# Kernel optimization log

Hardware: AMD Instinct MI355X
Metric: run time of the kernel (lower is better)

Reference implementation:

```python
import jax, jax.numpy as jnp
import numpy as np

V_WORD = 32000      # word vocab (dictionary.symbols minus specials)
NGRAM_VOCAB = 32001 # threshold top ngrams + UNK
DIM = 128
LATENT = 10000
NSPECIAL = 4
PAD_IDX = 1         # fairseq pad index
NG_PER_WORD = 26    # avg char-ngrams per word for n=4
B, T = 8, 1024


def setup_inputs() -> dict:
    key = jax.random.key(0)
    k1, k2, k3, k4, k5 = jax.random.split(key, 5)
    ngram_emb_weight = jax.random.normal(k1, (NGRAM_VOCAB, DIM), jnp.float32) * (DIM ** -0.5)
    latent_mat = jax.random.normal(k2, (LATENT, DIM), jnp.float32) * (LATENT ** -0.5)
    special_emb = jax.random.normal(k3, (NSPECIAL, DIM), jnp.float32) * (DIM ** -0.5)
    special_emb = special_emb.at[PAD_IDX].set(0.0)  # nn.init.constant_(special_emb[pad], 0)
    ngram_ids = jax.random.randint(k4, (V_WORD * NG_PER_WORD,), 0, NGRAM_VOCAB, jnp.int32)
    ngram_offsets = jnp.arange(V_WORD, dtype=jnp.int32) * NG_PER_WORD
    x = jax.random.randint(k5, (B, T), 0, NSPECIAL + V_WORD, jnp.int32)
    return {
        "ngram_emb_weight": ngram_emb_weight,
        "latent_mat": latent_mat,
        "special_emb": special_emb,
        "ngram_ids": ngram_ids,
        "ngram_offsets": ngram_offsets,
        "x": x,
    }


def reference(ngram_emb_weight, latent_mat, special_emb, ngram_ids, ngram_offsets, x):
    n_total = ngram_ids.shape[0]
    # EmbeddingBag(mode='sum'): segment-sum gathered ngram vectors per word
    seg = jnp.searchsorted(ngram_offsets, jnp.arange(n_total, dtype=ngram_offsets.dtype), side='right') - 1
    bag = jax.ops.segment_sum(ngram_emb_weight[ngram_ids], seg, num_segments=V_WORD)  # [V_WORD, DIM]
    lang_emb = jnp.tanh(bag)
    # softmax attention over the latent codebook
    latent_scores = jnp.einsum('vd,ld->vl', lang_emb, latent_mat)          # [V_WORD, LATENT]
    latent_distribution = jax.nn.softmax(latent_scores, axis=-1)
    latent_emb = jnp.einsum('vl,ld->vd', latent_distribution, latent_mat)  # [V_WORD, DIM]
    token_emb = lang_emb + latent_emb
    emb_weight = jnp.concatenate([special_emb, token_emb], axis=0)          # [NSPECIAL+V_WORD, DIM]
    sde_emb = emb_weight[x]                                                 # [B, T, DIM]
    return sde_emb
```

## Files before the change

kernel.cpp:

```cpp
#include <hip/hip_runtime.h>

typedef float  f32x4 __attribute__((ext_vector_type(4)));
typedef short  s16x8 __attribute__((ext_vector_type(8)));
typedef int    i32x4 __attribute__((ext_vector_type(4)));
typedef unsigned short u16x4 __attribute__((ext_vector_type(4)));
typedef unsigned int   u32x2 __attribute__((ext_vector_type(2)));

#define V_WORD   32000
#define DIM      128
#define LATENT   10000
#define LATP     10048
#define NSPECIAL 4
#define NTOK     8192
#define NTILE    157
#define BN       64
#define K0_BLOCKS 314

__device__ __forceinline__ unsigned short f2bf(float f) {
  unsigned u = __builtin_bit_cast(unsigned, f);
  unsigned r = (u + 0x7fffu + ((u >> 16) & 1u)) >> 16;
  return (unsigned short)r;
}

__device__ __forceinline__ unsigned cvt_pk_bf16(float lo, float hi) {
  unsigned r;
  asm("v_cvt_pk_bf16_f32 %0, %1, %2" : "=v"(r) : "v"(lo), "v"(hi));
  return r;
}

__device__ __forceinline__ float tanh_fast(float x) {
  float t = __expf(2.f * x);
  return (t - 1.f) * __frcp_rn(t + 1.f);
}

__device__ __forceinline__ void gload_lds16(const void* g, void* l) {
  __builtin_amdgcn_global_load_lds(
      (const __attribute__((address_space(1))) void*)g,
      (__attribute__((address_space(3))) void*)l, 16, 0, 0);
}

__global__ __launch_bounds__(256) void k01_prep(
    const float* __restrict__ latent, unsigned short* __restrict__ Lb,
    unsigned short* __restrict__ LTb,
    const float* __restrict__ ngram_emb, const int* __restrict__ ids,
    const int* __restrict__ offs, const int* __restrict__ x,
    float* __restrict__ langf, unsigned short* __restrict__ langb) {
  __shared__ float tile[32][129];
  int bid = blockIdx.x;
  int tid = threadIdx.x;
  if (bid < K0_BLOCKS) {
    int l0 = bid * 32;
    int r  = tid >> 3;
    int c0 = (tid & 7) * 16;
    int l  = l0 + r;
    for (int k = 0; k < 4; ++k) {
      int d = c0 + k * 4;
      f32x4 v = {0.f, 0.f, 0.f, 0.f};
      if (l < LATENT) v = *reinterpret_cast<const f32x4*>(latent + (size_t)l * DIM + d);
      tile[r][d + 0] = v[0]; tile[r][d + 1] = v[1];
      tile[r][d + 2] = v[2]; tile[r][d + 3] = v[3];
      u16x4 o = { f2bf(v[0]), f2bf(v[1]), f2bf(v[2]), f2bf(v[3]) };
      *reinterpret_cast<u16x4*>(Lb + (size_t)l * DIM + d) = o;
    }
    __syncthreads();
    int d = tid >> 1;
    int lbase = (tid & 1) * 16;
    for (int k = 0; k < 8; ++k) {
      int ll = lbase + 2 * k;
      int l1 = l0 + ll;
      unsigned pack = (unsigned)f2bf(tile[ll][d]) | ((unsigned)f2bf(tile[ll + 1][d]) << 16);
      *reinterpret_cast<unsigned*>(LTb + (size_t)d * LATP + l1) = pack;
    }
  } else {
    int tok  = (bid - K0_BLOCKS) * 4 + (tid >> 6);
    int lane = tid & 63;
    int half = lane >> 5;
    int l32  = lane & 31;
    int w = x[tok];
    f32x4 s0 = {0.f, 0.f, 0.f, 0.f}, s1 = {0.f, 0.f, 0.f, 0.f};
    if (w >= NSPECIAL) {
      int base = offs[w - NSPECIAL];
#pragma unroll
      for (int j = 0; j < 24; j += 4) {
        int ia = ids[base + j + half];
        int ib = ids[base + j + 2 + half];
        s0 += *reinterpret_cast<const f32x4*>(ngram_emb + (size_t)ia * DIM + l32 * 4);
        s1 += *reinterpret_cast<const f32x4*>(ngram_emb + (size_t)ib * DIM + l32 * 4);
      }
      int ic = ids[base + 24 + half];
      s0 += *reinterpret_cast<const f32x4*>(ngram_emb + (size_t)ic * DIM + l32 * 4);
      s0 += s1;
      for (int c = 0; c < 4; ++c) s0[c] += __shfl_xor(s0[c], 32, 64);
      for (int c = 0; c < 4; ++c) s0[c] = tanh_fast(s0[c]);
    }
    if (half == 0) {
      *reinterpret_cast<f32x4*>(langf + (size_t)tok * DIM + l32 * 4) = s0;
    } else {
      u32x2 pw = { cvt_pk_bf16(s0[0], s0[1]), cvt_pk_bf16(s0[2], s0[3]) };
      *reinterpret_cast<u32x2*>(langb + (size_t)tok * DIM + l32 * 4) = pw;
    }
  }
}

__global__ __launch_bounds__(256, 2) void k2_fused(
    const unsigned short* __restrict__ Lb,
    const unsigned short* __restrict__ LTb,
    const unsigned short* __restrict__ langb,
    float* __restrict__ Opart,
    float* __restrict__ Zpart,
    int nsplit) {
  __shared__ alignas(16) unsigned short smem[5 * 8192];
  unsigned short* Psh = smem + 4 * 8192;
  float* zsh = (float*)Psh;

  int bid = blockIdx.x;
  int xcd = bid & 7, idx = bid >> 3;
  int split, tokblk;
  if (nsplit == 8)      { split = xcd;                   tokblk = idx; }
  else if (nsplit == 16){ split = xcd * 2 + (idx >> 6);  tokblk = idx & 63; }
  else                  { split = xcd >> 1;              tokblk = idx + ((xcd & 1) << 5); }
  int tokbase = tokblk * 128;
  int t0 = (split * NTILE) / nsplit, t1 = ((split + 1) * NTILE) / nsplit;
  int lat_s = t0 * BN;
  int ntiles = t1 - t0;
  int npad = max(0, t1 * BN - LATENT);

  int tid = threadIdx.x;
  int wid = tid >> 6, lane = tid & 63;
  int lr = lane & 15, lg = lane >> 4;
  int wm = wid & 1, wn = wid >> 1;

  int rL  = tid >> 4, csL = tid & 15;
  int coL = csL ^ (rL & 7);
  int ddT = tid >> 3, csT = tid & 7;
  int coT = csT ^ (ddT & 7);
  const unsigned short* srcL0 = Lb + (size_t)rL * DIM + coL * 8;
  const unsigned short* srcT0 = LTb + (size_t)ddT * LATP + coT * 8;
  int wbase = wid * 64 * 8;

  auto issue = [&](int buf, int t) {
    int lat0 = lat_s + t * BN;
    const unsigned short* sL = srcL0 + (size_t)lat0 * DIM;
    const unsigned short* sT = srcT0 + lat0;
    unsigned short* dL = smem + buf * 8192 + wbase;
    unsigned short* dT = smem + 16384 + buf * 8192 + wbase;
#pragma unroll
    for (int i = 0; i < 4; ++i)
      gload_lds16(sL + (size_t)i * 16 * DIM, dL + i * 2048);
#pragma unroll
    for (int i = 0; i < 4; ++i)
      gload_lds16(sT + (size_t)i * 32 * LATP, dT + i * 2048);
  };

  s16x8 Bl[4][4];
  for (int n = 0; n < 4; ++n) {
    int row = tokbase + wn * 64 + n * 16 + lr;
    for (int kf = 0; kf < 4; ++kf)
      Bl[n][kf] = *reinterpret_cast<const s16x8*>(langb + (size_t)row * DIM + (kf * 4 + lg) * 8);
  }

  f32x4 acc2[4][4];
  for (int a = 0; a < 4; ++a)
    for (int b = 0; b < 4; ++b) acc2[a][b] = {0.f, 0.f, 0.f, 0.f};
  float zp[4] = {0.f, 0.f, 0.f, 0.f};

  issue(0, 0);
  int cur = 0;

  for (int t = 0; t < ntiles; ++t) {
    asm volatile("s_waitcnt vmcnt(0)" ::: "memory");
    __syncthreads();
    if (t + 1 < ntiles) issue(cur ^ 1, t + 1);

    const unsigned short* Lsh  = smem + cur * 8192;
    const unsigned short* LTsh = smem + 16384 + cur * 8192;

    f32x4 acc1[2][4];
    for (int m = 0; m < 2; ++m)
      for (int n = 0; n < 4; ++n) acc1[m][n] = {0.f, 0.f, 0.f, 0.f};
    for (int kf = 0; kf < 4; ++kf) {
      s16x8 a[2];
      for (int m = 0; m < 2; ++m) {
        int row = wm * 32 + m * 16 + lr;
        int c = kf * 4 + lg;
        a[m] = *reinterpret_cast<const s16x8*>(&Lsh[row * DIM + (c ^ (row & 7)) * 8]);
      }
      __builtin_amdgcn_s_setprio(1);
      for (int m = 0; m < 2; ++m)
        for (int n = 0; n < 4; ++n)
          acc1[m][n] = __builtin_amdgcn_mfma_f32_16x16x32_bf16(a[m], Bl[n][kf], acc1[m][n], 0, 0, 0);
      __builtin_amdgcn_s_setprio(0);
    }

    for (int m = 0; m < 2; ++m) {
      int la0 = wm * 32 + m * 16 + lg * 4;
      for (int n = 0; n < 4; ++n) {
        f32x4 v = acc1[m][n];
        float p0 = __expf(v[0]), p1 = __expf(v[1]);
        float p2 = __expf(v[2]), p3 = __expf(v[3]);
        zp[n] += p0; zp[n] += p1; zp[n] += p2; zp[n] += p3;
        u32x2 pw = { cvt_pk_bf16(p0, p1), cvt_pk_bf16(p2, p3) };
        int row = wn * 64 + n * 16 + lr;
        int c = la0 >> 3;
        *reinterpret_cast<u32x2*>(&Psh[row * 64 + ((c ^ (row & 7)) << 3) + (la0 & 7)]) = pw;
      }
    }
    __syncthreads();

    for (int kf = 0; kf < 2; ++kf) {
      s16x8 Ap[4], Bt[4];
      int c = kf * 4 + lg;
      for (int mr = 0; mr < 4; ++mr) {
        int row = wm * 64 + mr * 16 + lr;
        Ap[mr] = *reinterpret_cast<const s16x8*>(&Psh[row * 64 + ((c ^ (row & 7)) << 3)]);
      }
      for (int nd = 0; nd < 4; ++nd) {
        int dr = wn * 64 + nd * 16 + lr;
        Bt[nd] = *reinterpret_cast<const s16x8*>(&LTsh[dr * 64 + ((c ^ (dr & 7)) << 3)]);
      }
      __builtin_amdgcn_s_setprio(1);
      for (int mr = 0; mr < 4; ++mr)
        for (int nd = 0; nd < 4; ++nd)
          acc2[mr][nd] = __builtin_amdgcn_mfma_f32_16x16x32_bf16(Ap[mr], Bt[nd], acc2[mr][nd], 0, 0, 0);
      __builtin_amdgcn_s_setprio(0);
    }
    cur ^= 1;
  }

  __syncthreads();

  for (int n = 0; n < 4; ++n) {
    zp[n] += __shfl_xor(zp[n], 16, 64);
    zp[n] += __shfl_xor(zp[n], 32, 64);
  }
  if (wm == 0 && lane < 16)
    for (int n = 0; n < 4; ++n) zsh[wn * 64 + n * 16 + lr] = zp[n];
  __syncthreads();
  if (wm == 1 && lane < 16)
    for (int n = 0; n < 4; ++n) zsh[wn * 64 + n * 16 + lr] += zp[n];
  __syncthreads();

  for (int mr = 0; mr < 4; ++mr) {
    int rbase = wm * 64 + mr * 16 + lg * 4;
    for (int nd = 0; nd < 4; ++nd) {
      int dcol = wn * 64 + nd * 16 + lr;
      for (int i = 0; i < 4; ++i) {
        int row = rbase + i;
        Opart[((size_t)split * NTOK + tokbase + row) * DIM + dcol] = acc2[mr][nd][i];
      }
    }
  }
  if (tid < 128)
    Zpart[split * NTOK + tokbase + tid] = zsh[tid] - (float)npad;
}

__global__ __launch_bounds__(256) void k3_combine(
    const float* __restrict__ special, const int* __restrict__ x,
    const float* __restrict__ langf, const float* __restrict__ Opart,
    const float* __restrict__ Zpart, float* __restrict__ out, int nsplit) {
  int gi  = blockIdx.x * 256 + threadIdx.x;
  int tok = gi >> 5;
  int d4  = (gi & 31) * 4;
  int w   = x[tok];
  f32x4 o;
  if (w < NSPECIAL) {
    o = *reinterpret_cast<const f32x4*>(special + (size_t)w * DIM + d4);
  } else {
    f32x4 s = {0.f, 0.f, 0.f, 0.f};
    float z = 0.f;
    for (int sp = 0; sp < nsplit; ++sp) {
      s += *reinterpret_cast<const f32x4*>(Opart + ((size_t)sp * NTOK + tok) * DIM + d4);
      z += Zpart[sp * NTOK + tok];
    }
    f32x4 lg = *reinterpret_cast<const f32x4*>(langf + (size_t)tok * DIM + d4);
    o = lg + s / z;
  }
  *reinterpret_cast<f32x4*>(out + (size_t)tok * DIM + d4) = o;
}

extern "C" void kernel_launch(void* const* d_in, const int* in_sizes, int n_in,
                              void* d_out, int out_size, void* d_ws, size_t ws_size,
                              hipStream_t stream) {
  const float* ngram_emb = (const float*)d_in[0];
  const float* latent    = (const float*)d_in[1];
  const float* special   = (const float*)d_in[2];
  const int*   ids       = (const int*)d_in[3];
  const int*   offs      = (const int*)d_in[4];
  const int*   x         = (const int*)d_in[5];
  float* out = (float*)d_out;

  size_t fixed = (size_t)LATP * DIM * 2 * 2
               + (size_t)NTOK * DIM * 4
               + (size_t)NTOK * DIM * 2;
  int nsplit = 8;
  while (nsplit > 4) {
    size_t need = fixed + (size_t)nsplit * NTOK * DIM * 4 + (size_t)nsplit * NTOK * 4;
    if (need <= ws_size) break;
    nsplit >>= 1;
  }

  char* w = (char*)d_ws;
  unsigned short* Lb  = (unsigned short*)w;  w += (size_t)LATP * DIM * 2;
  unsigned short* LTb = (unsigned short*)w;  w += (size_t)DIM * LATP * 2;
  float* langf        = (float*)w;           w += (size_t)NTOK * DIM * 4;
  unsigned short* langb = (unsigned short*)w; w += (size_t)NTOK * DIM * 2;
  float* Opart        = (float*)w;           w += (size_t)nsplit * NTOK * DIM * 4;
  float* Zpart        = (float*)w;           w += (size_t)nsplit * NTOK * 4;

  hipLaunchKernelGGL(k01_prep, dim3(K0_BLOCKS + NTOK / 4), dim3(256), 0, stream,
                     latent, Lb, LTb, ngram_emb, ids, offs, x, langf, langb);
  hipLaunchKernelGGL(k2_fused, dim3(nsplit * 64), dim3(256), 0, stream,
                     Lb, LTb, langb, Opart, Zpart, nsplit);
  hipLaunchKernelGGL(k3_combine, dim3(NTOK * DIM / 4 / 256), dim3(256), 0, stream,
                     special, x, langf, Opart, Zpart, out, nsplit);
}
```

Before: 140.6 us.

## Shrink LDS footprint to fit three blocks per CU and raise split count

```diff
diff --git a/kernel.cpp b/kernel.cpp
--- a/kernel.cpp
+++ b/kernel.cpp
@@ -102,22 +102,21 @@
   }
 }
 
-__global__ __launch_bounds__(256, 2) void k2_fused(
+__global__ __launch_bounds__(256, 3) void k2_fused(
     const unsigned short* __restrict__ Lb,
     const unsigned short* __restrict__ LTb,
     const unsigned short* __restrict__ langb,
     float* __restrict__ Opart,
     float* __restrict__ Zpart,
     int nsplit) {
-  __shared__ alignas(16) unsigned short smem[5 * 8192];
-  unsigned short* Psh = smem + 4 * 8192;
-  float* zsh = (float*)Psh;
+  __shared__ alignas(16) unsigned short smem[3 * 8192];
+  __shared__ float zsh[128];
 
   int bid = blockIdx.x;
   int xcd = bid & 7, idx = bid >> 3;
   int split, tokblk;
-  if (nsplit == 8)      { split = xcd;                   tokblk = idx; }
-  else if (nsplit == 16){ split = xcd * 2 + (idx >> 6);  tokblk = idx & 63; }
+  if (nsplit == 16)     { split = xcd * 2 + (idx >> 6);  tokblk = idx & 63; }
+  else if (nsplit == 8) { split = xcd;                   tokblk = idx; }
   else                  { split = xcd >> 1;              tokblk = idx + ((xcd & 1) << 5); }
   int tokbase = tokblk * 128;
   int t0 = (split * NTILE) / nsplit, t1 = ((split + 1) * NTILE) / nsplit;
@@ -136,20 +135,23 @@
   int coT = csT ^ (ddT & 7);
   const unsigned short* srcL0 = Lb + (size_t)rL * DIM + coL * 8;
   const unsigned short* srcT0 = LTb + (size_t)ddT * LATP + coT * 8;
-  int wbase = wid * 64 * 8;
-
-  auto issue = [&](int buf, int t) {
-    int lat0 = lat_s + t * BN;
-    const unsigned short* sL = srcL0 + (size_t)lat0 * DIM;
-    const unsigned short* sT = srcT0 + lat0;
-    unsigned short* dL = smem + buf * 8192 + wbase;
-    unsigned short* dT = smem + 16384 + buf * 8192 + wbase;
+  int wbase = wid * 512;
+
+  unsigned short* LTsh = smem + 16384;
+
+  auto issue_L = [&](int buf, int t) {
+    const unsigned short* s = srcL0 + (size_t)(lat_s + t * BN) * DIM;
+    unsigned short* d = smem + buf * 8192 + wbase;
 #pragma unroll
     for (int i = 0; i < 4; ++i)
-      gload_lds16(sL + (size_t)i * 16 * DIM, dL + i * 2048);
+      gload_lds16(s + (size_t)i * 16 * DIM, d + i * 2048);
+  };
+  auto issue_LT = [&](int t) {
+    const unsigned short* s = srcT0 + (lat_s + t * BN);
+    unsigned short* d = LTsh + wbase;
 #pragma unroll
     for (int i = 0; i < 4; ++i)
-      gload_lds16(sT + (size_t)i * 32 * LATP, dT + i * 2048);
+      gload_lds16(s + (size_t)i * 32 * LATP, d + i * 2048);
   };
 
   s16x8 Bl[4][4];
@@ -164,16 +166,17 @@
     for (int b = 0; b < 4; ++b) acc2[a][b] = {0.f, 0.f, 0.f, 0.f};
   float zp[4] = {0.f, 0.f, 0.f, 0.f};
 
-  issue(0, 0);
+  issue_L(0, 0);
   int cur = 0;
 
   for (int t = 0; t < ntiles; ++t) {
+    bool more = (t + 1 < ntiles);
     asm volatile("s_waitcnt vmcnt(0)" ::: "memory");
     __syncthreads();
-    if (t + 1 < ntiles) issue(cur ^ 1, t + 1);
-
-    const unsigned short* Lsh  = smem + cur * 8192;
-    const unsigned short* LTsh = smem + 16384 + cur * 8192;
+    issue_LT(t);
+    if (more) issue_L(cur ^ 1, t + 1);
+
+    const unsigned short* Lsh = smem + cur * 8192;
 
     f32x4 acc1[2][4];
     for (int m = 0; m < 2; ++m)
@@ -191,7 +194,9 @@
           acc1[m][n] = __builtin_amdgcn_mfma_f32_16x16x32_bf16(a[m], Bl[n][kf], acc1[m][n], 0, 0, 0);
       __builtin_amdgcn_s_setprio(0);
     }
-
+    __syncthreads();
+
+    unsigned short* Psh = smem + cur * 8192;
     for (int m = 0; m < 2; ++m) {
       int la0 = wm * 32 + m * 16 + lg * 4;
       for (int n = 0; n < 4; ++n) {
@@ -205,6 +210,8 @@
         *reinterpret_cast<u32x2*>(&Psh[row * 64 + ((c ^ (row & 7)) << 3) + (la0 & 7)]) = pw;
       }
     }
+    if (more) asm volatile("s_waitcnt vmcnt(4)" ::: "memory");
+    else      asm volatile("s_waitcnt vmcnt(0)" ::: "memory");
     __syncthreads();
 
     for (int kf = 0; kf < 2; ++kf) {
@@ -227,12 +234,11 @@
     cur ^= 1;
   }
 
-  __syncthreads();
-
   for (int n = 0; n < 4; ++n) {
     zp[n] += __shfl_xor(zp[n], 16, 64);
     zp[n] += __shfl_xor(zp[n], 32, 64);
   }
+  __syncthreads();
   if (wm == 0 && lane < 16)
     for (int n = 0; n < 4; ++n) zsh[wn * 64 + n * 16 + lr] = zp[n];
   __syncthreads();
@@ -292,7 +298,7 @@
   size_t fixed = (size_t)LATP * DIM * 2 * 2
                + (size_t)NTOK * DIM * 4
                + (size_t)NTOK * DIM * 2;
-  int nsplit = 8;
+  int nsplit = 16;
   while (nsplit > 4) {
     size_t need = fixed + (size_t)nsplit * NTOK * DIM * 4 + (size_t)nsplit * NTOK * 4;
     if (need <= ws_size) break;
```

Measured after the change: 213.8 us. 52.1% more time.

## Fuse split-K combine into GEMM kernel via last-block atomic counter, store partials bf16

Applied to the files above, without the earlier changes.

```diff
diff --git a/kernel.cpp b/kernel.cpp
--- a/kernel.cpp
+++ b/kernel.cpp
@@ -14,6 +14,7 @@
 #define NTOK     8192
 #define NTILE    157
 #define BN       64
+#define NSPLIT   8
 #define K0_BLOCKS 314
 
 __device__ __forceinline__ unsigned short f2bf(float f) {
@@ -31,6 +32,13 @@
 __device__ __forceinline__ float tanh_fast(float x) {
   float t = __expf(2.f * x);
   return (t - 1.f) * __frcp_rn(t + 1.f);
+}
+
+__device__ __forceinline__ float bfl(unsigned u) {
+  return __builtin_bit_cast(float, u << 16);
+}
+__device__ __forceinline__ float bfh(unsigned u) {
+  return __builtin_bit_cast(float, u & 0xffff0000u);
 }
 
 __device__ __forceinline__ void gload_lds16(const void* g, void* l) {
@@ -44,10 +52,12 @@
     unsigned short* __restrict__ LTb,
     const float* __restrict__ ngram_emb, const int* __restrict__ ids,
     const int* __restrict__ offs, const int* __restrict__ x,
-    float* __restrict__ langf, unsigned short* __restrict__ langb) {
+    float* __restrict__ langf, unsigned short* __restrict__ langb,
+    int* __restrict__ cnt) {
   __shared__ float tile[32][129];
   int bid = blockIdx.x;
   int tid = threadIdx.x;
+  if (bid == 0 && tid < 64) cnt[tid] = 0;
   if (bid < K0_BLOCKS) {
     int l0 = bid * 32;
     int r  = tid >> 3;
@@ -106,21 +116,20 @@
     const unsigned short* __restrict__ Lb,
     const unsigned short* __restrict__ LTb,
     const unsigned short* __restrict__ langb,
-    float* __restrict__ Opart,
+    unsigned short* __restrict__ OpartB,
     float* __restrict__ Zpart,
-    int nsplit) {
+    int* __restrict__ cnt,
+    const float* __restrict__ special, const int* __restrict__ x,
+    const float* __restrict__ langf, float* __restrict__ outp) {
   __shared__ alignas(16) unsigned short smem[5 * 8192];
   unsigned short* Psh = smem + 4 * 8192;
   float* zsh = (float*)Psh;
 
   int bid = blockIdx.x;
   int xcd = bid & 7, idx = bid >> 3;
-  int split, tokblk;
-  if (nsplit == 8)      { split = xcd;                   tokblk = idx; }
-  else if (nsplit == 16){ split = xcd * 2 + (idx >> 6);  tokblk = idx & 63; }
-  else                  { split = xcd >> 1;              tokblk = idx + ((xcd & 1) << 5); }
+  int split = xcd, tokblk = idx;
   int tokbase = tokblk * 128;
-  int t0 = (split * NTILE) / nsplit, t1 = ((split + 1) * NTILE) / nsplit;
+  int t0 = (split * NTILE) / NSPLIT, t1 = ((split + 1) * NTILE) / NSPLIT;
   int lat_s = t0 * BN;
   int ntiles = t1 - t0;
   int npad = max(0, t1 * BN - LATENT);
@@ -136,7 +145,7 @@
   int coT = csT ^ (ddT & 7);
   const unsigned short* srcL0 = Lb + (size_t)rL * DIM + coL * 8;
   const unsigned short* srcT0 = LTb + (size_t)ddT * LATP + coT * 8;
-  int wbase = wid * 64 * 8;
+  int wbase = wid * 512;
 
   auto issue = [&](int buf, int t) {
     int lat0 = lat_s + t * BN;
@@ -246,36 +255,58 @@
       int dcol = wn * 64 + nd * 16 + lr;
       for (int i = 0; i < 4; ++i) {
         int row = rbase + i;
-        Opart[((size_t)split * NTOK + tokbase + row) * DIM + dcol] = acc2[mr][nd][i];
+        OpartB[((size_t)split * NTOK + tokbase + row) * DIM + dcol] = f2bf(acc2[mr][nd][i]);
       }
     }
   }
   if (tid < 128)
     Zpart[split * NTOK + tokbase + tid] = zsh[tid] - (float)npad;
-}
-
-__global__ __launch_bounds__(256) void k3_combine(
-    const float* __restrict__ special, const int* __restrict__ x,
-    const float* __restrict__ langf, const float* __restrict__ Opart,
-    const float* __restrict__ Zpart, float* __restrict__ out, int nsplit) {
-  int gi  = blockIdx.x * 256 + threadIdx.x;
-  int tok = gi >> 5;
-  int d4  = (gi & 31) * 4;
-  int w   = x[tok];
-  f32x4 o;
-  if (w < NSPECIAL) {
-    o = *reinterpret_cast<const f32x4*>(special + (size_t)w * DIM + d4);
-  } else {
-    f32x4 s = {0.f, 0.f, 0.f, 0.f};
-    float z = 0.f;
-    for (int sp = 0; sp < nsplit; ++sp) {
-      s += *reinterpret_cast<const f32x4*>(Opart + ((size_t)sp * NTOK + tok) * DIM + d4);
-      z += Zpart[sp * NTOK + tok];
-    }
-    f32x4 lg = *reinterpret_cast<const f32x4*>(langf + (size_t)tok * DIM + d4);
-    o = lg + s / z;
-  }
-  *reinterpret_cast<f32x4*>(out + (size_t)tok * DIM + d4) = o;
+
+  __threadfence();
+  __syncthreads();
+  int* sflag = (int*)(zsh + 128);
+  if (tid == 0) *sflag = atomicAdd(&cnt[tokblk], 1);
+  __syncthreads();
+  if (*sflag == NSPLIT - 1) {
+    __threadfence();
+    int tk = tokbase + (tid >> 1);
+    int dh = (tid & 1) * 64;
+    int w  = x[tk];
+    if (w < NSPECIAL) {
+#pragma unroll
+      for (int c = 0; c < 16; ++c)
+        *reinterpret_cast<f32x4*>(outp + (size_t)tk * DIM + dh + c * 4) =
+            *reinterpret_cast<const f32x4*>(special + (size_t)w * DIM + dh + c * 4);
+    } else {
+      float z = 0.f;
+#pragma unroll
+      for (int sp = 0; sp < NSPLIT; ++sp) z += Zpart[sp * NTOK + tk];
+      float rz = 1.0f / z;
+#pragma unroll
+      for (int c = 0; c < 8; ++c) {
+        float acc[8] = {0.f, 0.f, 0.f, 0.f, 0.f, 0.f, 0.f, 0.f};
+#pragma unroll
+        for (int sp = 0; sp < NSPLIT; ++sp) {
+          i32x4 v = *reinterpret_cast<const i32x4*>(
+              OpartB + ((size_t)sp * NTOK + tk) * DIM + dh + c * 8);
+#pragma unroll
+          for (int e = 0; e < 4; ++e) {
+            unsigned u = (unsigned)v[e];
+            acc[2 * e]     += bfl(u);
+            acc[2 * e + 1] += bfh(u);
+          }
+        }
+        f32x4 lgA = *reinterpret_cast<const f32x4*>(langf + (size_t)tk * DIM + dh + c * 8);
+        f32x4 lgB = *reinterpret_cast<const f32x4*>(langf + (size_t)tk * DIM + dh + c * 8 + 4);
+        f32x4 oA = { lgA[0] + acc[0] * rz, lgA[1] + acc[1] * rz,
+                     lgA[2] + acc[2] * rz, lgA[3] + acc[3] * rz };
+        f32x4 oB = { lgB[0] + acc[4] * rz, lgB[1] + acc[5] * rz,
+                     lgB[2] + acc[6] * rz, lgB[3] + acc[7] * rz };
+        *reinterpret_cast<f32x4*>(outp + (size_t)tk * DIM + dh + c * 8) = oA;
+        *reinterpret_cast<f32x4*>(outp + (size_t)tk * DIM + dh + c * 8 + 4) = oB;
+      }
+    }
+  }
 }
 
 extern "C" void kernel_launch(void* const* d_in, const int* in_sizes, int n_in,
@@ -289,28 +320,17 @@
   const int*   x         = (const int*)d_in[5];
   float* out = (float*)d_out;
 
-  size_t fixed = (size_t)LATP * DIM * 2 * 2
-               + (size_t)NTOK * DIM * 4
-               + (size_t)NTOK * DIM * 2;
-  int nsplit = 8;
-  while (nsplit > 4) {
-    size_t need = fixed + (size_t)nsplit * NTOK * DIM * 4 + (size_t)nsplit * NTOK * 4;
-    if (need <= ws_size) break;
-    nsplit >>= 1;
-  }
-
   char* w = (char*)d_ws;
   unsigned short* Lb  = (unsigned short*)w;  w += (size_t)LATP * DIM * 2;
   unsigned short* LTb = (unsigned short*)w;  w += (size_t)DIM * LATP * 2;
   float* langf        = (float*)w;           w += (size_t)NTOK * DIM * 4;
   unsigned short* langb = (unsigned short*)w; w += (size_t)NTOK * DIM * 2;
-  float* Opart        = (float*)w;           w += (size_t)nsplit * NTOK * DIM * 4;
-  float* Zpart        = (float*)w;           w += (size_t)nsplit * NTOK * 4;
+  unsigned short* OpartB = (unsigned short*)w; w += (size_t)NSPLIT * NTOK * DIM * 2;
+  float* Zpart        = (float*)w;           w += (size_t)NSPLIT * NTOK * 4;
+  int* cnt            = (int*)w;             w += 64 * 4;
 
   hipLaunchKernelGGL(k01_prep, dim3(K0_BLOCKS + NTOK / 4), dim3(256), 0, stream,
-                     latent, Lb, LTb, ngram_emb, ids, offs, x, langf, langb);
-  hipLaunchKernelGGL(k2_fused, dim3(nsplit * 64), dim3(256), 0, stream,
-                     Lb, LTb, langb, Opart, Zpart, nsplit);
-  hipLaunchKernelGGL(k3_combine, dim3(NTOK * DIM / 4 / 256), dim3(256), 0, stream,
-                     special, x, langf, Opart, Zpart, out, nsplit);
-}
+                     latent, Lb, LTb, ngram_emb, ids, offs, x, langf, langb, cnt);
+  hipLaunchKernelGGL(k2_fused, dim3(NSPLIT * 64), dim3(256), 0, stream,
+                     Lb, LTb, langb, OpartB, Zpart, cnt, special, x, langf, out);
+}
```

After: 251.9 us. 79.1% more time.
